# Optimization experiments

Measured on AMD Instinct MI355X. Metric: run time of the kernel, lower is better.

Reference implementation:

```python
import jax, jax.numpy as jnp
import numpy as np

BN_EPS = 1e-5
N_NODES = 100000
N_EDGES = 1600000
IN_DIM = 128
HID = 256   # 2 * out_dim
OUT_DIM = 128


def setup_inputs() -> dict:
    key = jax.random.key(0)
    ks = jax.random.split(key, 8)
    x = jax.random.normal(ks[0], (N_NODES, IN_DIM), dtype=jnp.float32)
    edge_index = jax.random.randint(ks[1], (2, N_EDGES), 0, N_NODES, dtype=jnp.int32)
    # GINConv learned eps (train_eps=True), init 0
    eps = jnp.zeros((), dtype=jnp.float32)
    # MLP: Linear(in, 2*out) -> BN -> ReLU -> Linear(2*out, out)
    s1 = 1.0 / np.sqrt(IN_DIM)
    s2 = 1.0 / np.sqrt(HID)
    W1 = jax.random.uniform(ks[2], (IN_DIM, HID), jnp.float32, -s1, s1)
    b1 = jax.random.uniform(ks[3], (HID,), jnp.float32, -s1, s1)
    g1 = jnp.ones((HID,), jnp.float32)
    beta1 = jnp.zeros((HID,), jnp.float32)
    W2 = jax.random.uniform(ks[4], (HID, OUT_DIM), jnp.float32, -s2, s2)
    b2 = jax.random.uniform(ks[5], (OUT_DIM,), jnp.float32, -s2, s2)
    # outer BatchNorm
    g2 = jnp.ones((OUT_DIM,), jnp.float32)
    beta2 = jnp.zeros((OUT_DIM,), jnp.float32)
    return {"x": x, "edge_index": edge_index, "eps": eps,
            "W1": W1, "b1": b1, "g1": g1, "beta1": beta1,
            "W2": W2, "b2": b2, "g2": g2, "beta2": beta2}


def _batchnorm(h, gamma, beta):
    # training-mode BatchNorm1d: batch mean, biased variance
    mu = jnp.mean(h, axis=0)
    var = jnp.mean(jnp.square(h - mu), axis=0)
    return (h - mu) * jax.lax.rsqrt(var + BN_EPS) * gamma + beta


def reference(x, edge_index, eps, W1, b1, g1, beta1, W2, b2, g2, beta2):
    src, dst = edge_index[0], edge_index[1]
    # sum-aggregation of neighbor features: scatter-add x[src] onto dst
    aggr = jax.ops.segment_sum(x[src], dst, num_segments=x.shape[0])  # [N, in_dim]
    h = (1.0 + eps) * x + aggr
    # MLP: Linear -> BN -> ReLU -> Linear
    h = h @ W1 + b1
    h = jax.nn.relu(_batchnorm(h, g1, beta1))
    h = h @ W2 + b2
    # outer BN + ReLU
    return jax.nn.relu(_batchnorm(h, g2, beta2))
```

## Files before the change

### kernel.cpp

```cpp
#include <hip/hip_runtime.h>
#include <hip/hip_bf16.h>

#define N_NODES 100000
#define N_EDGES 1600000
#define IN_DIM  128
#define HID     256
#define OUT_DIM 128
#define BN_EPS  1e-5f

typedef unsigned int u32;
typedef unsigned short u16;
typedef __attribute__((ext_vector_type(8))) short short8v;
typedef __attribute__((ext_vector_type(4))) float f32x4;

__device__ __forceinline__ float bf2f(u16 h) {
    return __uint_as_float(((u32)h) << 16);
}
__device__ __forceinline__ u16 f2bf(float f) {
    u32 u = __float_as_uint(f);
    u32 r = (u + 0x7fffu + ((u >> 16) & 1u)) >> 16;
    return (u16)r;
}
__device__ __forceinline__ u32 pack2(float a, float b) {
    return (u32)f2bf(a) | ((u32)f2bf(b) << 16);
}
__device__ __forceinline__ void gload16(const void* g, void* l) {
    __builtin_amdgcn_global_load_lds((const __attribute__((address_space(1))) u32*)g,
                                     (__attribute__((address_space(3))) u32*)l, 16, 0, 0);
}
#define MFMA(a,b,c) __builtin_amdgcn_mfma_f32_16x16x32_bf16(a, b, c, 0, 0, 0)

__global__ __launch_bounds__(256) void k_prep(const float* __restrict__ x,
                                              const int* __restrict__ ei,
                                              const float* __restrict__ W1,
                                              const float* __restrict__ W2,
                                              uint2* __restrict__ xb,
                                              int* __restrict__ head2,
                                              int2* __restrict__ nxt,
                                              char* __restrict__ w1t,
                                              char* __restrict__ w2t) {
    int t = blockIdx.x * 256 + threadIdx.x;
    {
        float4 v = ((const float4*)x)[t];
        uint2 p;
        p.x = pack2(v.x, v.y);
        p.y = pack2(v.z, v.w);
        xb[t] = p;
    }
    if (t < N_EDGES) {
        int dst = ei[N_EDGES + t];
        int src = ei[t];
        int old = atomicExch(&head2[dst * 2 + (t & 1)], t);
        nxt[t] = make_int2(old, src);
    }
    if (t < 8192) {
        u16 tmp[8];
        if (t < 4096) {
            int j = t >> 4, kc = t & 15;
            #pragma unroll
            for (int i = 0; i < 8; ++i) tmp[i] = f2bf(W1[(kc * 8 + i) * HID + j]);
            u32 off = ((u32)(j * 256 + kc * 16)) ^ (((u32)(j & 7)) << 4);
            uint4 q;
            q.x = (u32)tmp[0] | ((u32)tmp[1] << 16);
            q.y = (u32)tmp[2] | ((u32)tmp[3] << 16);
            q.z = (u32)tmp[4] | ((u32)tmp[5] << 16);
            q.w = (u32)tmp[6] | ((u32)tmp[7] << 16);
            *(uint4*)(w1t + off) = q;
        } else {
            int t2 = t - 4096;
            int j = t2 >> 5, kc = t2 & 31;
            #pragma unroll
            for (int i = 0; i < 8; ++i) tmp[i] = f2bf(W2[(kc * 8 + i) * OUT_DIM + j]);
            u32 off = ((u32)(j * 512 + kc * 16)) ^ (((u32)(j & 7)) << 4);
            uint4 q;
            q.x = (u32)tmp[0] | ((u32)tmp[1] << 16);
            q.y = (u32)tmp[2] | ((u32)tmp[3] << 16);
            q.z = (u32)tmp[4] | ((u32)tmp[5] << 16);
            q.w = (u32)tmp[6] | ((u32)tmp[7] << 16);
            *(uint4*)(w2t + off) = q;
        }
    }
}

__global__ __launch_bounds__(256) void k_aggregate(const uint4* __restrict__ xb4,
                                                   const int2* __restrict__ nxt,
                                                   const int* __restrict__ head2,
                                                   const float* __restrict__ epsp,
                                                   char* __restrict__ aggrb) {
    const int lane = threadIdx.x & 63;
    const int w = threadIdx.x >> 6;
    const int q = lane >> 4, l = lane & 15;
    const int nq = q >> 1, p = q & 1;
    const int node = blockIdx.x * 8 + w * 2 + nq;

    float a[8];
    #pragma unroll
    for (int i = 0; i < 8; ++i) a[i] = 0.f;

    if (p == 0) {
        float sc = 1.0f + epsp[0];
        uint4 v = xb4[node * 16 + l];
        a[0] = bf2f((u16)v.x) * sc;  a[1] = bf2f((u16)(v.x >> 16)) * sc;
        a[2] = bf2f((u16)v.y) * sc;  a[3] = bf2f((u16)(v.y >> 16)) * sc;
        a[4] = bf2f((u16)v.z) * sc;  a[5] = bf2f((u16)(v.z >> 16)) * sc;
        a[6] = bf2f((u16)v.w) * sc;  a[7] = bf2f((u16)(v.w >> 16)) * sc;
    }
    int e = head2[node * 2 + p];
    while (e >= 0) {
        int2 nv = nxt[e];
        e = nv.x;
        uint4 v = xb4[nv.y * 16 + l];
        a[0] += bf2f((u16)v.x);  a[1] += bf2f((u16)(v.x >> 16));
        a[2] += bf2f((u16)v.y);  a[3] += bf2f((u16)(v.y >> 16));
        a[4] += bf2f((u16)v.z);  a[5] += bf2f((u16)(v.z >> 16));
        a[6] += bf2f((u16)v.w);  a[7] += bf2f((u16)(v.w >> 16));
    }
    #pragma unroll
    for (int i = 0; i < 8; ++i) a[i] += __shfl_xor(a[i], 16);
    if (p == 0) {
        uint4 o;
        o.x = pack2(a[0], a[1]);
        o.y = pack2(a[2], a[3]);
        o.z = pack2(a[4], a[5]);
        o.w = pack2(a[6], a[7]);
        u32 b = ((u32)node * 256 + (u32)l * 16) ^ (((u32)(node & 7)) << 4);
        *(uint4*)(aggrb + b) = o;
    }
}

__global__ __launch_bounds__(512) void k_gemm1(const char* __restrict__ aggrb,
                                               const char* __restrict__ w1t,
                                               const float* __restrict__ b1,
                                               u16* __restrict__ h1t,
                                               float* __restrict__ gstats) {
    __shared__ u16 Als[160 * 128];
    __shared__ u16 Bls[256 * 128];
    __shared__ float slds[512];

    const int tid = threadIdx.x, lane = tid & 63, w = tid >> 6;
    const int wr = w >> 2, wc = w & 3;
    const int base = blockIdx.x * 160;

    slds[tid] = 0.f;

    char* lA = (char*)Als;
    char* lB = (char*)Bls;
    const char* ga = aggrb + (size_t)base * 256;
    #pragma unroll
    for (int i = 0; i < 5; ++i)
        gload16(ga + i * 8192 + w * 1024 + (lane << 4), lA + i * 8192 + w * 1024);
    #pragma unroll
    for (int i = 0; i < 8; ++i)
        gload16(w1t + i * 8192 + w * 1024 + (lane << 4), lB + i * 8192 + w * 1024);

    const int rA = lane & 15;
    const int q = lane >> 4;
    const int kb = q << 3;
    const u32 xsw = ((u32)(rA & 7)) << 4;
    int colv[4]; float bcol[4];
    #pragma unroll
    for (int n = 0; n < 4; ++n) { colv[n] = wc * 64 + n * 16 + rA; bcol[n] = b1[colv[n]]; }

    asm volatile("s_waitcnt vmcnt(0)" ::: "memory");
    __syncthreads();

    f32x4 acc[5][4];
    #pragma unroll
    for (int m = 0; m < 5; ++m)
        #pragma unroll
        for (int n = 0; n < 4; ++n) acc[m][n] = (f32x4){0.f, 0.f, 0.f, 0.f};

    #pragma unroll
    for (int ks = 0; ks < 4; ++ks) {
        const int kk2 = (ks * 32 + kb) * 2;
        short8v a[5], b[4];
        #pragma unroll
        for (int m = 0; m < 5; ++m) {
            u32 off = ((u32)((wr * 80 + m * 16 + rA) * 256 + kk2)) ^ xsw;
            a[m] = *(const short8v*)(lA + off);
        }
        #pragma unroll
        for (int n = 0; n < 4; ++n) {
            u32 off = ((u32)(colv[n] * 256 + kk2)) ^ xsw;
            b[n] = *(const short8v*)(lB + off);
        }
        #pragma unroll
        for (int m = 0; m < 5; ++m)
            #pragma unroll
            for (int n = 0; n < 4; ++n)
                acc[m][n] = MFMA(a[m], b[n], acc[m][n]);
    }

    const int Tb = blockIdx.x * 10 + wr * 5;
    float csum[4] = {0.f,0.f,0.f,0.f}, csq[4] = {0.f,0.f,0.f,0.f};
    #pragma unroll
    for (int m = 0; m < 5; ++m) {
        int T = Tb + m;
        #pragma unroll
        for (int n = 0; n < 4; ++n) {
            f32x4 d = acc[m][n];
            float v0 = d[0] + bcol[n], v1 = d[1] + bcol[n];
            float v2 = d[2] + bcol[n], v3 = d[3] + bcol[n];
            csum[n] += v0 + v1 + v2 + v3;
            csq[n]  += v0*v0 + v1*v1 + v2*v2 + v3*v3;
            uint2 p; p.x = pack2(v0, v1); p.y = pack2(v2, v3);
            *(uint2*)(h1t + (size_t)T * 4096 + colv[n] * 16 + q * 4) = p;
        }
    }
    #pragma unroll
    for (int n = 0; n < 4; ++n) {
        csum[n] += __shfl_xor(csum[n], 16); csum[n] += __shfl_xor(csum[n], 32);
        csq[n]  += __shfl_xor(csq[n], 16);  csq[n]  += __shfl_xor(csq[n], 32);
    }
    if (lane < 16) {
        #pragma unroll
        for (int n = 0; n < 4; ++n) {
            atomicAdd(&slds[colv[n]], csum[n]);
            atomicAdd(&slds[256 + colv[n]], csq[n]);
        }
    }
    __syncthreads();
    atomicAdd(&gstats[tid], slds[tid]);
}

__global__ __launch_bounds__(512) void k_gemm2(const uint4* __restrict__ h1t4,
                                               const char* __restrict__ w2t,
                                               const float* __restrict__ b2,
                                               const float* __restrict__ g1,
                                               const float* __restrict__ beta1,
                                               const float* __restrict__ gstats,
                                               u16* __restrict__ h2t,
                                               float* __restrict__ gstats2) {
    __shared__ u16 Als[160 * 128];
    __shared__ u16 Bls[128 * 256];
    __shared__ float a1s[256], b1s[256];
    __shared__ float slds[256];

    const int tid = threadIdx.x, lane = tid & 63, w = tid >> 6;
    const int wr = w >> 2, wc = w & 3;
    const int Tbase = blockIdx.x * 10;

    if (tid < 256) {
        float s = gstats[tid], sq = gstats[256 + tid];
        float mu = s * (1.0f / N_NODES);
        float var = sq * (1.0f / N_NODES) - mu * mu;
        float inv = rsqrtf(var + BN_EPS);
        float a = g1[tid] * inv;
        a1s[tid] = a;
        b1s[tid] = beta1[tid] - mu * a;
        slds[tid] = 0.f;
    }

    char* lA = (char*)Als;
    char* lB = (char*)Bls;
    #pragma unroll
    for (int i = 0; i < 8; ++i)
        gload16(w2t + i * 8192 + w * 1024 + (lane << 4), lB + i * 8192 + w * 1024);

    const int rA = lane & 15;
    const int q = lane >> 4;
    const int kb = q << 3;
    const u32 xsw = ((u32)(rA & 7)) << 4;
    int colv[2]; float bcol[2];
    #pragma unroll
    for (int n = 0; n < 2; ++n) { colv[n] = wc * 32 + n * 16 + rA; bcol[n] = b2[colv[n]]; }

    __syncthreads();

    f32x4 acc[5][2];
    #pragma unroll
    for (int m = 0; m < 5; ++m)
        #pragma unroll
        for (int n = 0; n < 2; ++n) acc[m][n] = (f32x4){0.f, 0.f, 0.f, 0.f};

    for (int kh = 0; kh < 2; ++kh) {
        #pragma unroll
        for (int i = 0; i < 5; ++i) {
            int id = i * 512 + tid;
            int kl = id & 127;
            int h16 = (id >> 7) & 1;
            int Tl = id >> 8;
            int kg = kh * 128 + kl;
            uint4 v = h1t4[(size_t)(Tbase + Tl) * 512 + kg * 2 + h16];
            float a = a1s[kg], b = b1s[kg];
            int r0 = Tl * 16 + h16 * 8;
            u16 hv[8] = {(u16)v.x, (u16)(v.x >> 16), (u16)v.y, (u16)(v.y >> 16),
                         (u16)v.z, (u16)(v.z >> 16), (u16)v.w, (u16)(v.w >> 16)};
            #pragma unroll
            for (int rr = 0; rr < 8; ++rr) {
                float f = fmaxf(bf2f(hv[rr]) * a + b, 0.f);
                int r = r0 + rr;
                u32 off = ((u32)(r * 256 + kl * 2)) ^ (((u32)(r & 7)) << 4);
                *(u16*)(lA + off) = f2bf(f);
            }
        }
        if (kh == 0) asm volatile("s_waitcnt vmcnt(0)" ::: "memory");
        __syncthreads();

        #pragma unroll
        for (int ks = 0; ks < 4; ++ks) {
            const int kk2 = (ks * 32 + kb) * 2;
            short8v a[5], b[2];
            #pragma unroll
            for (int n = 0; n < 2; ++n) {
                u32 off = ((u32)(colv[n] * 512 + kh * 256 + kk2)) ^ xsw;
                b[n] = *(const short8v*)(lB + off);
            }
            #pragma unroll
            for (int m = 0; m < 5; ++m) {
                u32 off = ((u32)((wr * 80 + m * 16 + rA) * 256 + kk2)) ^ xsw;
                a[m] = *(const short8v*)(lA + off);
            }
            #pragma unroll
            for (int m = 0; m < 5; ++m)
                #pragma unroll
                for (int n = 0; n < 2; ++n)
                    acc[m][n] = MFMA(a[m], b[n], acc[m][n]);
        }
        __syncthreads();
    }

    const int Tb = Tbase + wr * 5;
    float csum[2] = {0.f,0.f}, csq[2] = {0.f,0.f};
    #pragma unroll
    for (int m = 0; m < 5; ++m) {
        int T = Tb + m;
        #pragma unroll
        for (int n = 0; n < 2; ++n) {
            f32x4 d = acc[m][n];
            float v0 = d[0] + bcol[n], v1 = d[1] + bcol[n];
            float v2 = d[2] + bcol[n], v3 = d[3] + bcol[n];
            csum[n] += v0 + v1 + v2 + v3;
            csq[n]  += v0*v0 + v1*v1 + v2*v2 + v3*v3;
            uint2 p; p.x = pack2(v0, v1); p.y = pack2(v2, v3);
            *(uint2*)(h2t + (size_t)T * 2048 + colv[n] * 16 + q * 4) = p;
        }
    }
    #pragma unroll
    for (int n = 0; n < 2; ++n) {
        csum[n] += __shfl_xor(csum[n], 16); csum[n] += __shfl_xor(csum[n], 32);
        csq[n]  += __shfl_xor(csq[n], 16);  csq[n]  += __shfl_xor(csq[n], 32);
    }
    if (lane < 16) {
        #pragma unroll
        for (int n = 0; n < 2; ++n) {
            atomicAdd(&slds[colv[n]], csum[n]);
            atomicAdd(&slds[128 + colv[n]], csq[n]);
        }
    }
    __syncthreads();
    if (tid < 256) atomicAdd(&gstats2[tid], slds[tid]);
}

__global__ __launch_bounds__(256) void k_bn2(const uint4* __restrict__ h2t4,
                                             float* __restrict__ out,
                                             const float* __restrict__ gstats2,
                                             const float* __restrict__ g2,
                                             const float* __restrict__ beta2) {
    __shared__ float fl[32 * 128];
    __shared__ float a2s[128], b2s[128];
    const int tid = threadIdx.x;
    if (tid < 128) {
        float s = gstats2[tid], sq = gstats2[128 + tid];
        float mu = s * (1.0f / N_NODES);
        float var = sq * (1.0f / N_NODES) - mu * mu;
        float inv = rsqrtf(var + BN_EPS);
        float a = g2[tid] * inv;
        a2s[tid] = a;
        b2s[tid] = beta2[tid] - mu * a;
    }
    __syncthreads();
    const int Tbase = blockIdx.x * 2;
    #pragma unroll
    for (int i = 0; i < 2; ++i) {
        int id = i * 256 + tid;
        int kl = id & 127;
        int h16 = (id >> 7) & 1;
        int Tl = id >> 8;
        uint4 v = h2t4[(size_t)(Tbase + Tl) * 256 + kl * 2 + h16];
        float a = a2s[kl], b = b2s[kl];
        int r0 = Tl * 16 + h16 * 8;
        u16 hv[8] = {(u16)v.x, (u16)(v.x >> 16), (u16)v.y, (u16)(v.y >> 16),
                     (u16)v.z, (u16)(v.z >> 16), (u16)v.w, (u16)(v.w >> 16)};
        #pragma unroll
        for (int rr = 0; rr < 8; ++rr)
            fl[(r0 + rr) * 128 + kl] = fmaxf(bf2f(hv[rr]) * a + b, 0.f);
    }
    __syncthreads();
    #pragma unroll
    for (int i = 0; i < 4; ++i) {
        int id = i * 256 + tid;
        int row = id >> 5;
        int ch = id & 31;
        float4 vv = *(const float4*)&fl[row * 128 + ch * 4];
        ((float4*)out)[(size_t)(blockIdx.x * 32 + row) * 32 + ch] = vv;
    }
}

extern "C" void kernel_launch(void* const* d_in, const int* in_sizes, int n_in,
                              void* d_out, int out_size, void* d_ws, size_t ws_size,
                              hipStream_t stream) {
    const float* x     = (const float*)d_in[0];
    const int*   ei    = (const int*)d_in[1];
    const float* epsp  = (const float*)d_in[2];
    const float* W1    = (const float*)d_in[3];
    const float* b1    = (const float*)d_in[4];
    const float* g1    = (const float*)d_in[5];
    const float* beta1 = (const float*)d_in[6];
    const float* W2    = (const float*)d_in[7];
    const float* b2    = (const float*)d_in[8];
    const float* g2    = (const float*)d_in[9];
    const float* beta2 = (const float*)d_in[10];

    char* ws = (char*)d_ws;
    char*  aggrb   = ws;
    u16*   h2t     = (u16*)ws;
    u16*   h1t     = (u16*)(ws + 25600000);
    int2*  nxt     = (int2*)(ws + 25600000);
    int*   head2   = (int*)(ws + 38400000);
    uint2* xb      = (uint2*)(ws + 39200000);
    float* gstats  = (float*)(ws + 76800000);
    float* gstats2 = gstats + 512;
    char*  w1t     = ws + 76804096;
    char*  w2t     = ws + 76869632;
    float* out = (float*)d_out;

    hipMemsetAsync(head2, 0xFF, 800000, stream);
    hipMemsetAsync(gstats, 0, 768 * sizeof(float), stream);

    k_prep<<<12500, 256, 0, stream>>>(x, ei, W1, W2, xb, head2, nxt, w1t, w2t);
    k_aggregate<<<N_NODES / 8, 256, 0, stream>>>((const uint4*)xb, nxt, head2, epsp, aggrb);
    k_gemm1<<<625, 512, 0, stream>>>(aggrb, w1t, b1, h1t, gstats);
    k_gemm2<<<625, 512, 0, stream>>>((const uint4*)h1t, w2t, b2, g1, beta1, gstats, h2t, gstats2);
    k_bn2<<<3125, 256, 0, stream>>>((const uint4*)h2t, out, gstats2, g2, beta2);
}
```

Before: 257.0 us.

## Halve GEMM weight LDS via K-split loads, restructure aggregation, fold stats memset

Weight tiles in both GEMM kernels are now staged into LDS in two K-halves instead of all at once. This halves the B buffer, so more blocks can be resident per CU, at the cost of an extra barrier and a serialized weight load per half. The aggregation kernel now assigns one 16-lane group per node, which walks both edge lists with two interleaved chains, removing the cross-group shuffle and halving thread count. Zeroing of the BN stats buffer moves into the prep kernel, removing one memset launch.

```diff
diff --git a/kernel.cpp b/kernel.cpp
--- a/kernel.cpp
+++ b/kernel.cpp
@@ -38,7 +38,8 @@
                                               int* __restrict__ head2,
                                               int2* __restrict__ nxt,
                                               char* __restrict__ w1t,
-                                              char* __restrict__ w2t) {
+                                              char* __restrict__ w2t,
+                                              float* __restrict__ gstats) {
     int t = blockIdx.x * 256 + threadIdx.x;
     {
         float4 v = ((const float4*)x)[t];
@@ -53,6 +54,7 @@
         int old = atomicExch(&head2[dst * 2 + (t & 1)], t);
         nxt[t] = make_int2(old, src);
     }
+    if (t < 768) gstats[t] = 0.f;
     if (t < 8192) {
         u16 tmp[8];
         if (t < 4096) {
@@ -87,45 +89,60 @@
                                                    const int* __restrict__ head2,
                                                    const float* __restrict__ epsp,
                                                    char* __restrict__ aggrb) {
-    const int lane = threadIdx.x & 63;
-    const int w = threadIdx.x >> 6;
-    const int q = lane >> 4, l = lane & 15;
-    const int nq = q >> 1, p = q & 1;
-    const int node = blockIdx.x * 8 + w * 2 + nq;
-
+    const int tid = threadIdx.x;
+    const int l = tid & 15;
+    const int node = blockIdx.x * 16 + (tid >> 4);
+
+    const float sc = 1.0f + epsp[0];
+    uint4 v = xb4[node * 16 + l];
     float a[8];
-    #pragma unroll
-    for (int i = 0; i < 8; ++i) a[i] = 0.f;
-
-    if (p == 0) {
-        float sc = 1.0f + epsp[0];
-        uint4 v = xb4[node * 16 + l];
-        a[0] = bf2f((u16)v.x) * sc;  a[1] = bf2f((u16)(v.x >> 16)) * sc;
-        a[2] = bf2f((u16)v.y) * sc;  a[3] = bf2f((u16)(v.y >> 16)) * sc;
-        a[4] = bf2f((u16)v.z) * sc;  a[5] = bf2f((u16)(v.z >> 16)) * sc;
-        a[6] = bf2f((u16)v.w) * sc;  a[7] = bf2f((u16)(v.w >> 16)) * sc;
-    }
-    int e = head2[node * 2 + p];
-    while (e >= 0) {
-        int2 nv = nxt[e];
-        e = nv.x;
-        uint4 v = xb4[nv.y * 16 + l];
-        a[0] += bf2f((u16)v.x);  a[1] += bf2f((u16)(v.x >> 16));
-        a[2] += bf2f((u16)v.y);  a[3] += bf2f((u16)(v.y >> 16));
-        a[4] += bf2f((u16)v.z);  a[5] += bf2f((u16)(v.z >> 16));
-        a[6] += bf2f((u16)v.w);  a[7] += bf2f((u16)(v.w >> 16));
-    }
-    #pragma unroll
-    for (int i = 0; i < 8; ++i) a[i] += __shfl_xor(a[i], 16);
-    if (p == 0) {
-        uint4 o;
-        o.x = pack2(a[0], a[1]);
-        o.y = pack2(a[2], a[3]);
-        o.z = pack2(a[4], a[5]);
-        o.w = pack2(a[6], a[7]);
-        u32 b = ((u32)node * 256 + (u32)l * 16) ^ (((u32)(node & 7)) << 4);
-        *(uint4*)(aggrb + b) = o;
-    }
+    a[0] = bf2f((u16)v.x) * sc;  a[1] = bf2f((u16)(v.x >> 16)) * sc;
+    a[2] = bf2f((u16)v.y) * sc;  a[3] = bf2f((u16)(v.y >> 16)) * sc;
+    a[4] = bf2f((u16)v.z) * sc;  a[5] = bf2f((u16)(v.z >> 16)) * sc;
+    a[6] = bf2f((u16)v.w) * sc;  a[7] = bf2f((u16)(v.w >> 16)) * sc;
+
+    int e0 = head2[node * 2];
+    int e1 = head2[node * 2 + 1];
+    while (e0 >= 0 && e1 >= 0) {
+        int2 n0 = nxt[e0];
+        int2 n1 = nxt[e1];
+        uint4 v0 = xb4[n0.y * 16 + l];
+        uint4 v1 = xb4[n1.y * 16 + l];
+        e0 = n0.x; e1 = n1.x;
+        a[0] += bf2f((u16)v0.x);  a[1] += bf2f((u16)(v0.x >> 16));
+        a[2] += bf2f((u16)v0.y);  a[3] += bf2f((u16)(v0.y >> 16));
+        a[4] += bf2f((u16)v0.z);  a[5] += bf2f((u16)(v0.z >> 16));
+        a[6] += bf2f((u16)v0.w);  a[7] += bf2f((u16)(v0.w >> 16));
+        a[0] += bf2f((u16)v1.x);  a[1] += bf2f((u16)(v1.x >> 16));
+        a[2] += bf2f((u16)v1.y);  a[3] += bf2f((u16)(v1.y >> 16));
+        a[4] += bf2f((u16)v1.z);  a[5] += bf2f((u16)(v1.z >> 16));
+        a[6] += bf2f((u16)v1.w);  a[7] += bf2f((u16)(v1.w >> 16));
+    }
+    while (e0 >= 0) {
+        int2 n0 = nxt[e0];
+        uint4 v0 = xb4[n0.y * 16 + l];
+        e0 = n0.x;
+        a[0] += bf2f((u16)v0.x);  a[1] += bf2f((u16)(v0.x >> 16));
+        a[2] += bf2f((u16)v0.y);  a[3] += bf2f((u16)(v0.y >> 16));
+        a[4] += bf2f((u16)v0.z);  a[5] += bf2f((u16)(v0.z >> 16));
+        a[6] += bf2f((u16)v0.w);  a[7] += bf2f((u16)(v0.w >> 16));
+    }
+    while (e1 >= 0) {
+        int2 n1 = nxt[e1];
+        uint4 v1 = xb4[n1.y * 16 + l];
+        e1 = n1.x;
+        a[0] += bf2f((u16)v1.x);  a[1] += bf2f((u16)(v1.x >> 16));
+        a[2] += bf2f((u16)v1.y);  a[3] += bf2f((u16)(v1.y >> 16));
+        a[4] += bf2f((u16)v1.z);  a[5] += bf2f((u16)(v1.z >> 16));
+        a[6] += bf2f((u16)v1.w);  a[7] += bf2f((u16)(v1.w >> 16));
+    }
+    uint4 o;
+    o.x = pack2(a[0], a[1]);
+    o.y = pack2(a[2], a[3]);
+    o.z = pack2(a[4], a[5]);
+    o.w = pack2(a[6], a[7]);
+    u32 b = ((u32)node * 256 + (u32)l * 16) ^ (((u32)(node & 7)) << 4);
+    *(uint4*)(aggrb + b) = o;
 }
 
 __global__ __launch_bounds__(512) void k_gemm1(const char* __restrict__ aggrb,
@@ -134,7 +151,7 @@
                                                u16* __restrict__ h1t,
                                                float* __restrict__ gstats) {
     __shared__ u16 Als[160 * 128];
-    __shared__ u16 Bls[256 * 128];
+    __shared__ u16 Bls[256 * 64];
     __shared__ float slds[512];
 
     const int tid = threadIdx.x, lane = tid & 63, w = tid >> 6;
@@ -149,9 +166,6 @@
     #pragma unroll
     for (int i = 0; i < 5; ++i)
         gload16(ga + i * 8192 + w * 1024 + (lane << 4), lA + i * 8192 + w * 1024);
-    #pragma unroll
-    for (int i = 0; i < 8; ++i)
-        gload16(w1t + i * 8192 + w * 1024 + (lane << 4), lB + i * 8192 + w * 1024);
 
     const int rA = lane & 15;
     const int q = lane >> 4;
@@ -161,34 +175,45 @@
     #pragma unroll
     for (int n = 0; n < 4; ++n) { colv[n] = wc * 64 + n * 16 + rA; bcol[n] = b1[colv[n]]; }
 
-    asm volatile("s_waitcnt vmcnt(0)" ::: "memory");
-    __syncthreads();
-
     f32x4 acc[5][4];
     #pragma unroll
     for (int m = 0; m < 5; ++m)
         #pragma unroll
         for (int n = 0; n < 4; ++n) acc[m][n] = (f32x4){0.f, 0.f, 0.f, 0.f};
 
-    #pragma unroll
-    for (int ks = 0; ks < 4; ++ks) {
-        const int kk2 = (ks * 32 + kb) * 2;
-        short8v a[5], b[4];
-        #pragma unroll
-        for (int m = 0; m < 5; ++m) {
-            u32 off = ((u32)((wr * 80 + m * 16 + rA) * 256 + kk2)) ^ xsw;
-            a[m] = *(const short8v*)(lA + off);
-        }
-        #pragma unroll
-        for (int n = 0; n < 4; ++n) {
-            u32 off = ((u32)(colv[n] * 256 + kk2)) ^ xsw;
-            b[n] = *(const short8v*)(lB + off);
-        }
-        #pragma unroll
-        for (int m = 0; m < 5; ++m)
-            #pragma unroll
-            for (int n = 0; n < 4; ++n)
-                acc[m][n] = MFMA(a[m], b[n], acc[m][n]);
+    for (int kh = 0; kh < 2; ++kh) {
+        if (kh) __syncthreads();
+        #pragma unroll
+        for (int i = 0; i < 4; ++i) {
+            int idx = i * 512 + tid;
+            int j = idx >> 3, kc8 = idx & 7;
+            u32 src = (u32)j * 256 + (u32)kh * 128 + (u32)kc8 * 16;
+            gload16(w1t + src, lB + idx * 16);
+        }
+        asm volatile("s_waitcnt vmcnt(0)" ::: "memory");
+        __syncthreads();
+
+        #pragma unroll
+        for (int ksl = 0; ksl < 2; ++ksl) {
+            const int kk2A = (kh * 64 + ksl * 32 + kb) * 2;
+            const int kk2B = (ksl * 32 + kb) * 2;
+            short8v a[5], b[4];
+            #pragma unroll
+            for (int m = 0; m < 5; ++m) {
+                u32 off = ((u32)((wr * 80 + m * 16 + rA) * 256 + kk2A)) ^ xsw;
+                a[m] = *(const short8v*)(lA + off);
+            }
+            #pragma unroll
+            for (int n = 0; n < 4; ++n) {
+                u32 off = ((u32)(colv[n] * 128 + kk2B)) ^ xsw;
+                b[n] = *(const short8v*)(lB + off);
+            }
+            #pragma unroll
+            for (int m = 0; m < 5; ++m)
+                #pragma unroll
+                for (int n = 0; n < 4; ++n)
+                    acc[m][n] = MFMA(a[m], b[n], acc[m][n]);
+        }
     }
 
     const int Tb = blockIdx.x * 10 + wr * 5;
@@ -232,7 +257,7 @@
                                                u16* __restrict__ h2t,
                                                float* __restrict__ gstats2) {
     __shared__ u16 Als[160 * 128];
-    __shared__ u16 Bls[128 * 256];
+    __shared__ u16 Bls[128 * 128];
     __shared__ float a1s[256], b1s[256];
     __shared__ float slds[256];
 
@@ -253,9 +278,6 @@
 
     char* lA = (char*)Als;
     char* lB = (char*)Bls;
-    #pragma unroll
-    for (int i = 0; i < 8; ++i)
-        gload16(w2t + i * 8192 + w * 1024 + (lane << 4), lB + i * 8192 + w * 1024);
 
     const int rA = lane & 15;
     const int q = lane >> 4;
@@ -294,7 +316,14 @@
                 *(u16*)(lA + off) = f2bf(f);
             }
         }
-        if (kh == 0) asm volatile("s_waitcnt vmcnt(0)" ::: "memory");
+        #pragma unroll
+        for (int i = 0; i < 4; ++i) {
+            int idx = i * 512 + tid;
+            int j = idx >> 4, kc16 = idx & 15;
+            u32 src = (u32)j * 512 + (u32)kh * 256 + (u32)kc16 * 16;
+            gload16(w2t + src, lB + idx * 16);
+        }
+        asm volatile("s_waitcnt vmcnt(0)" ::: "memory");
         __syncthreads();
 
         #pragma unroll
@@ -303,7 +332,7 @@
             short8v a[5], b[2];
             #pragma unroll
             for (int n = 0; n < 2; ++n) {
-                u32 off = ((u32)(colv[n] * 512 + kh * 256 + kk2)) ^ xsw;
+                u32 off = ((u32)(colv[n] * 256 + kk2)) ^ xsw;
                 b[n] = *(const short8v*)(lB + off);
             }
             #pragma unroll
@@ -426,10 +455,9 @@
     float* out = (float*)d_out;
 
     hipMemsetAsync(head2, 0xFF, 800000, stream);
-    hipMemsetAsync(gstats, 0, 768 * sizeof(float), stream);
-
-    k_prep<<<12500, 256, 0, stream>>>(x, ei, W1, W2, xb, head2, nxt, w1t, w2t);
-    k_aggregate<<<N_NODES / 8, 256, 0, stream>>>((const uint4*)xb, nxt, head2, epsp, aggrb);
+
+    k_prep<<<12500, 256, 0, stream>>>(x, ei, W1, W2, xb, head2, nxt, w1t, w2t, gstats);
+    k_aggregate<<<N_NODES / 16, 256, 0, stream>>>((const uint4*)xb, nxt, head2, epsp, aggrb);
     k_gemm1<<<625, 512, 0, stream>>>(aggrb, w1t, b1, h1t, gstats);
     k_gemm2<<<625, 512, 0, stream>>>((const uint4*)h1t, w2t, b2, g1, beta1, gstats, h2t, gstats2);
     k_bn2<<<3125, 256, 0, stream>>>((const uint4*)h2t, out, gstats2, g2, beta2);
```

Measured after the change: 253.3 us. Within noise of the previous version (-1.4%).

## Halve GEMM tiles and stage weights in K-chunks for higher occupancy

Applied to the files above, without the earlier changes.

Both GEMM kernels drop from 160-row tiles with 512 threads to 80-row tiles with 256 threads and twice as many blocks. The weight matrix is now staged through LDS in K-chunks, which shrinks shared memory so more blocks fit per CU, with launch_bounds occupancy hints added. Block-level LDS stat reduction is replaced by direct global atomics, and the gstats memset moves into k_prep. In exchange there are more barriers, repeated weight loads per block, and more global atomic traffic.

```diff
diff --git a/kernel.cpp b/kernel.cpp
--- a/kernel.cpp
+++ b/kernel.cpp
@@ -38,7 +38,8 @@
                                               int* __restrict__ head2,
                                               int2* __restrict__ nxt,
                                               char* __restrict__ w1t,
-                                              char* __restrict__ w2t) {
+                                              char* __restrict__ w2t,
+                                              float* __restrict__ gstats) {
     int t = blockIdx.x * 256 + threadIdx.x;
     {
         float4 v = ((const float4*)x)[t];
@@ -53,6 +54,7 @@
         int old = atomicExch(&head2[dst * 2 + (t & 1)], t);
         nxt[t] = make_int2(old, src);
     }
+    if (t < 768) gstats[t] = 0.f;
     if (t < 8192) {
         u16 tmp[8];
         if (t < 4096) {
@@ -128,70 +130,72 @@
     }
 }
 
-__global__ __launch_bounds__(512) void k_gemm1(const char* __restrict__ aggrb,
-                                               const char* __restrict__ w1t,
-                                               const float* __restrict__ b1,
-                                               u16* __restrict__ h1t,
-                                               float* __restrict__ gstats) {
-    __shared__ u16 Als[160 * 128];
-    __shared__ u16 Bls[256 * 128];
-    __shared__ float slds[512];
-
-    const int tid = threadIdx.x, lane = tid & 63, w = tid >> 6;
-    const int wr = w >> 2, wc = w & 3;
-    const int base = blockIdx.x * 160;
-
-    slds[tid] = 0.f;
-
-    char* lA = (char*)Als;
-    char* lB = (char*)Bls;
-    const char* ga = aggrb + (size_t)base * 256;
-    #pragma unroll
-    for (int i = 0; i < 5; ++i)
-        gload16(ga + i * 8192 + w * 1024 + (lane << 4), lA + i * 8192 + w * 1024);
-    #pragma unroll
-    for (int i = 0; i < 8; ++i)
-        gload16(w1t + i * 8192 + w * 1024 + (lane << 4), lB + i * 8192 + w * 1024);
-
+__global__ __launch_bounds__(256, 3) void k_gemm1(const char* __restrict__ aggrb,
+                                                  const char* __restrict__ w1t,
+                                                  const float* __restrict__ b1,
+                                                  u16* __restrict__ h1t,
+                                                  float* __restrict__ gstats) {
+    __shared__ u16 Als[80 * 128];
+    __shared__ u16 Bls[256 * 64];
+
+    const int tid = threadIdx.x, lane = tid & 63, wc = tid >> 6;
     const int rA = lane & 15;
     const int q = lane >> 4;
     const int kb = q << 3;
     const u32 xsw = ((u32)(rA & 7)) << 4;
+
+    char* lA = (char*)Als;
+    char* lB = (char*)Bls;
+    const char* ga = aggrb + (size_t)blockIdx.x * 20480;
+    #pragma unroll
+    for (int i = 0; i < 5; ++i)
+        gload16(ga + (i * 256 + tid) * 16, lA + (i * 256 + tid) * 16);
+
     int colv[4]; float bcol[4];
     #pragma unroll
     for (int n = 0; n < 4; ++n) { colv[n] = wc * 64 + n * 16 + rA; bcol[n] = b1[colv[n]]; }
 
-    asm volatile("s_waitcnt vmcnt(0)" ::: "memory");
-    __syncthreads();
-
     f32x4 acc[5][4];
     #pragma unroll
     for (int m = 0; m < 5; ++m)
         #pragma unroll
         for (int n = 0; n < 4; ++n) acc[m][n] = (f32x4){0.f, 0.f, 0.f, 0.f};
 
-    #pragma unroll
-    for (int ks = 0; ks < 4; ++ks) {
-        const int kk2 = (ks * 32 + kb) * 2;
-        short8v a[5], b[4];
-        #pragma unroll
-        for (int m = 0; m < 5; ++m) {
-            u32 off = ((u32)((wr * 80 + m * 16 + rA) * 256 + kk2)) ^ xsw;
-            a[m] = *(const short8v*)(lA + off);
-        }
-        #pragma unroll
-        for (int n = 0; n < 4; ++n) {
-            u32 off = ((u32)(colv[n] * 256 + kk2)) ^ xsw;
-            b[n] = *(const short8v*)(lB + off);
-        }
-        #pragma unroll
-        for (int m = 0; m < 5; ++m)
-            #pragma unroll
-            for (int n = 0; n < 4; ++n)
-                acc[m][n] = MFMA(a[m], b[n], acc[m][n]);
-    }
-
-    const int Tb = blockIdx.x * 10 + wr * 5;
+    for (int kh = 0; kh < 2; ++kh) {
+        if (kh) __syncthreads();
+        #pragma unroll
+        for (int i = 0; i < 8; ++i) {
+            int idx = i * 256 + tid;
+            int j = idx >> 3, kc8 = idx & 7;
+            gload16(w1t + (u32)j * 256 + (u32)kh * 128 + (u32)kc8 * 16, lB + idx * 16);
+        }
+        asm volatile("s_waitcnt vmcnt(0)" ::: "memory");
+        __syncthreads();
+
+        #pragma unroll
+        for (int ksl = 0; ksl < 2; ++ksl) {
+            const int kk2A = (kh * 64 + ksl * 32 + kb) * 2;
+            const int kk2B = (ksl * 32 + kb) * 2;
+            short8v a[5], b[4];
+            #pragma unroll
+            for (int m = 0; m < 5; ++m) {
+                u32 off = ((u32)((m * 16 + rA) * 256 + kk2A)) ^ xsw;
+                a[m] = *(const short8v*)(lA + off);
+            }
+            #pragma unroll
+            for (int n = 0; n < 4; ++n) {
+                u32 off = ((u32)(colv[n] * 128 + kk2B)) ^ xsw;
+                b[n] = *(const short8v*)(lB + off);
+            }
+            #pragma unroll
+            for (int m = 0; m < 5; ++m)
+                #pragma unroll
+                for (int n = 0; n < 4; ++n)
+                    acc[m][n] = MFMA(a[m], b[n], acc[m][n]);
+        }
+    }
+
+    const int Tb = blockIdx.x * 5;
     float csum[4] = {0.f,0.f,0.f,0.f}, csq[4] = {0.f,0.f,0.f,0.f};
     #pragma unroll
     for (int m = 0; m < 5; ++m) {
@@ -215,32 +219,32 @@
     if (lane < 16) {
         #pragma unroll
         for (int n = 0; n < 4; ++n) {
-            atomicAdd(&slds[colv[n]], csum[n]);
-            atomicAdd(&slds[256 + colv[n]], csq[n]);
-        }
-    }
-    __syncthreads();
-    atomicAdd(&gstats[tid], slds[tid]);
-}
-
-__global__ __launch_bounds__(512) void k_gemm2(const uint4* __restrict__ h1t4,
-                                               const char* __restrict__ w2t,
-                                               const float* __restrict__ b2,
-                                               const float* __restrict__ g1,
-                                               const float* __restrict__ beta1,
-                                               const float* __restrict__ gstats,
-                                               u16* __restrict__ h2t,
-                                               float* __restrict__ gstats2) {
-    __shared__ u16 Als[160 * 128];
-    __shared__ u16 Bls[128 * 256];
+            atomicAdd(&gstats[colv[n]], csum[n]);
+            atomicAdd(&gstats[256 + colv[n]], csq[n]);
+        }
+    }
+}
+
+__global__ __launch_bounds__(256, 4) void k_gemm2(const uint4* __restrict__ h1t4,
+                                                  const char* __restrict__ w2t,
+                                                  const float* __restrict__ b2,
+                                                  const float* __restrict__ g1,
+                                                  const float* __restrict__ beta1,
+                                                  const float* __restrict__ gstats,
+                                                  u16* __restrict__ h2t,
+                                                  float* __restrict__ gstats2) {
+    __shared__ u16 Als[80 * 128];
+    __shared__ u16 Bls[128 * 64];
     __shared__ float a1s[256], b1s[256];
-    __shared__ float slds[256];
-
-    const int tid = threadIdx.x, lane = tid & 63, w = tid >> 6;
-    const int wr = w >> 2, wc = w & 3;
-    const int Tbase = blockIdx.x * 10;
-
-    if (tid < 256) {
+
+    const int tid = threadIdx.x, lane = tid & 63, wc = tid >> 6;
+    const int rA = lane & 15;
+    const int q = lane >> 4;
+    const int kb = q << 3;
+    const u32 xsw = ((u32)(rA & 7)) << 4;
+    const int Tbase = blockIdx.x * 5;
+
+    {
         float s = gstats[tid], sq = gstats[256 + tid];
         float mu = s * (1.0f / N_NODES);
         float var = sq * (1.0f / N_NODES) - mu * mu;
@@ -248,19 +252,10 @@
         float a = g1[tid] * inv;
         a1s[tid] = a;
         b1s[tid] = beta1[tid] - mu * a;
-        slds[tid] = 0.f;
     }
 
     char* lA = (char*)Als;
     char* lB = (char*)Bls;
-    #pragma unroll
-    for (int i = 0; i < 8; ++i)
-        gload16(w2t + i * 8192 + w * 1024 + (lane << 4), lB + i * 8192 + w * 1024);
-
-    const int rA = lane & 15;
-    const int q = lane >> 4;
-    const int kb = q << 3;
-    const u32 xsw = ((u32)(rA & 7)) << 4;
     int colv[2]; float bcol[2];
     #pragma unroll
     for (int n = 0; n < 2; ++n) { colv[n] = wc * 32 + n * 16 + rA; bcol[n] = b2[colv[n]]; }
@@ -276,7 +271,7 @@
     for (int kh = 0; kh < 2; ++kh) {
         #pragma unroll
         for (int i = 0; i < 5; ++i) {
-            int id = i * 512 + tid;
+            int id = i * 256 + tid;
             int kl = id & 127;
             int h16 = (id >> 7) & 1;
             int Tl = id >> 8;
@@ -294,37 +289,46 @@
                 *(u16*)(lA + off) = f2bf(f);
             }
         }
-        if (kh == 0) asm volatile("s_waitcnt vmcnt(0)" ::: "memory");
-        __syncthreads();
-
-        #pragma unroll
-        for (int ks = 0; ks < 4; ++ks) {
-            const int kk2 = (ks * 32 + kb) * 2;
-            short8v a[5], b[2];
-            #pragma unroll
-            for (int n = 0; n < 2; ++n) {
-                u32 off = ((u32)(colv[n] * 512 + kh * 256 + kk2)) ^ xsw;
-                b[n] = *(const short8v*)(lB + off);
+        for (int kq = 0; kq < 2; ++kq) {
+            #pragma unroll
+            for (int i = 0; i < 4; ++i) {
+                int idx = i * 256 + tid;
+                int j = idx >> 3, kc8 = idx & 7;
+                gload16(w2t + (u32)j * 512 + (u32)(kh * 2 + kq) * 128 + (u32)kc8 * 16,
+                        lB + idx * 16);
             }
-            #pragma unroll
-            for (int m = 0; m < 5; ++m) {
-                u32 off = ((u32)((wr * 80 + m * 16 + rA) * 256 + kk2)) ^ xsw;
-                a[m] = *(const short8v*)(lA + off);
+            asm volatile("s_waitcnt vmcnt(0)" ::: "memory");
+            __syncthreads();
+
+            #pragma unroll
+            for (int ks = 0; ks < 2; ++ks) {
+                const int kk2A = (kq * 64 + ks * 32 + kb) * 2;
+                const int kk2B = (ks * 32 + kb) * 2;
+                short8v a[5], b[2];
+                #pragma unroll
+                for (int n = 0; n < 2; ++n) {
+                    u32 off = ((u32)(colv[n] * 128 + kk2B)) ^ xsw;
+                    b[n] = *(const short8v*)(lB + off);
+                }
+                #pragma unroll
+                for (int m = 0; m < 5; ++m) {
+                    u32 off = ((u32)((m * 16 + rA) * 256 + kk2A)) ^ xsw;
+                    a[m] = *(const short8v*)(lA + off);
+                }
+                #pragma unroll
+                for (int m = 0; m < 5; ++m)
+                    #pragma unroll
+                    for (int n = 0; n < 2; ++n)
+                        acc[m][n] = MFMA(a[m], b[n], acc[m][n]);
             }
-            #pragma unroll
-            for (int m = 0; m < 5; ++m)
-                #pragma unroll
-                for (int n = 0; n < 2; ++n)
-                    acc[m][n] = MFMA(a[m], b[n], acc[m][n]);
-        }
-        __syncthreads();
-    }
-
-    const int Tb = Tbase + wr * 5;
+            __syncthreads();
+        }
+    }
+
     float csum[2] = {0.f,0.f}, csq[2] = {0.f,0.f};
     #pragma unroll
     for (int m = 0; m < 5; ++m) {
-        int T = Tb + m;
+        int T = Tbase + m;
         #pragma unroll
         for (int n = 0; n < 2; ++n) {
             f32x4 d = acc[m][n];
@@ -344,12 +348,10 @@
     if (lane < 16) {
         #pragma unroll
         for (int n = 0; n < 2; ++n) {
-            atomicAdd(&slds[colv[n]], csum[n]);
-            atomicAdd(&slds[128 + colv[n]], csq[n]);
-        }
-    }
-    __syncthreads();
-    if (tid < 256) atomicAdd(&gstats2[tid], slds[tid]);
+            atomicAdd(&gstats2[colv[n]], csum[n]);
+            atomicAdd(&gstats2[128 + colv[n]], csq[n]);
+        }
+    }
 }
 
 __global__ __launch_bounds__(256) void k_bn2(const uint4* __restrict__ h2t4,
@@ -426,11 +428,10 @@
     float* out = (float*)d_out;
 
     hipMemsetAsync(head2, 0xFF, 800000, stream);
-    hipMemsetAsync(gstats, 0, 768 * sizeof(float), stream);
-
-    k_prep<<<12500, 256, 0, stream>>>(x, ei, W1, W2, xb, head2, nxt, w1t, w2t);
+
+    k_prep<<<12500, 256, 0, stream>>>(x, ei, W1, W2, xb, head2, nxt, w1t, w2t, gstats);
     k_aggregate<<<N_NODES / 8, 256, 0, stream>>>((const uint4*)xb, nxt, head2, epsp, aggrb);
-    k_gemm1<<<625, 512, 0, stream>>>(aggrb, w1t, b1, h1t, gstats);
-    k_gemm2<<<625, 512, 0, stream>>>((const uint4*)h1t, w2t, b2, g1, beta1, gstats, h2t, gstats2);
+    k_gemm1<<<1250, 256, 0, stream>>>(aggrb, w1t, b1, h1t, gstats);
+    k_gemm2<<<1250, 256, 0, stream>>>((const uint4*)h1t, w2t, b2, g1, beta1, gstats, h2t, gstats2);
     k_bn2<<<3125, 256, 0, stream>>>((const uint4*)h2t, out, gstats2, g2, beta2);
 }
```

New measurement: 298.2 us. 1.16x slower.

## Read GEMM weight tiles directly from global memory and fold stats zeroing into prep

Applied to the files above, without the earlier changes.

Both GEMM kernels stop staging the bf16 weight matrices in LDS and read B fragments straight from global memory (L2/L1-cached), so the weight layout drops its XOR swizzle. This cuts LDS use per block (64KB less), which may allow more resident blocks, and removes the bulk weight copy at the start of each block. In exchange, every MFMA step issues global loads with higher latency. The zeroing of the BN statistics buffer moves from a separate memset into the prep kernel, removing one launch.

```diff
diff --git a/kernel.cpp b/kernel.cpp
--- a/kernel.cpp
+++ b/kernel.cpp
@@ -38,7 +38,8 @@
                                               int* __restrict__ head2,
                                               int2* __restrict__ nxt,
                                               char* __restrict__ w1t,
-                                              char* __restrict__ w2t) {
+                                              char* __restrict__ w2t,
+                                              float* __restrict__ gstats) {
     int t = blockIdx.x * 256 + threadIdx.x;
     {
         float4 v = ((const float4*)x)[t];
@@ -53,13 +54,14 @@
         int old = atomicExch(&head2[dst * 2 + (t & 1)], t);
         nxt[t] = make_int2(old, src);
     }
+    if (t < 768) gstats[t] = 0.f;
     if (t < 8192) {
         u16 tmp[8];
         if (t < 4096) {
             int j = t >> 4, kc = t & 15;
             #pragma unroll
             for (int i = 0; i < 8; ++i) tmp[i] = f2bf(W1[(kc * 8 + i) * HID + j]);
-            u32 off = ((u32)(j * 256 + kc * 16)) ^ (((u32)(j & 7)) << 4);
+            u32 off = (u32)(j * 256 + kc * 16);
             uint4 q;
             q.x = (u32)tmp[0] | ((u32)tmp[1] << 16);
             q.y = (u32)tmp[2] | ((u32)tmp[3] << 16);
@@ -71,7 +73,7 @@
             int j = t2 >> 5, kc = t2 & 31;
             #pragma unroll
             for (int i = 0; i < 8; ++i) tmp[i] = f2bf(W2[(kc * 8 + i) * OUT_DIM + j]);
-            u32 off = ((u32)(j * 512 + kc * 16)) ^ (((u32)(j & 7)) << 4);
+            u32 off = (u32)(j * 512 + kc * 16);
             uint4 q;
             q.x = (u32)tmp[0] | ((u32)tmp[1] << 16);
             q.y = (u32)tmp[2] | ((u32)tmp[3] << 16);
@@ -134,7 +136,6 @@
                                                u16* __restrict__ h1t,
                                                float* __restrict__ gstats) {
     __shared__ u16 Als[160 * 128];
-    __shared__ u16 Bls[256 * 128];
     __shared__ float slds[512];
 
     const int tid = threadIdx.x, lane = tid & 63, w = tid >> 6;
@@ -144,14 +145,10 @@
     slds[tid] = 0.f;
 
     char* lA = (char*)Als;
-    char* lB = (char*)Bls;
     const char* ga = aggrb + (size_t)base * 256;
     #pragma unroll
     for (int i = 0; i < 5; ++i)
         gload16(ga + i * 8192 + w * 1024 + (lane << 4), lA + i * 8192 + w * 1024);
-    #pragma unroll
-    for (int i = 0; i < 8; ++i)
-        gload16(w1t + i * 8192 + w * 1024 + (lane << 4), lB + i * 8192 + w * 1024);
 
     const int rA = lane & 15;
     const int q = lane >> 4;
@@ -175,14 +172,12 @@
         const int kk2 = (ks * 32 + kb) * 2;
         short8v a[5], b[4];
         #pragma unroll
+        for (int n = 0; n < 4; ++n)
+            b[n] = *(const short8v*)(w1t + colv[n] * 256 + kk2);
+        #pragma unroll
         for (int m = 0; m < 5; ++m) {
             u32 off = ((u32)((wr * 80 + m * 16 + rA) * 256 + kk2)) ^ xsw;
             a[m] = *(const short8v*)(lA + off);
-        }
-        #pragma unroll
-        for (int n = 0; n < 4; ++n) {
-            u32 off = ((u32)(colv[n] * 256 + kk2)) ^ xsw;
-            b[n] = *(const short8v*)(lB + off);
         }
         #pragma unroll
         for (int m = 0; m < 5; ++m)
@@ -232,7 +227,6 @@
                                                u16* __restrict__ h2t,
                                                float* __restrict__ gstats2) {
     __shared__ u16 Als[160 * 128];
-    __shared__ u16 Bls[128 * 256];
     __shared__ float a1s[256], b1s[256];
     __shared__ float slds[256];
 
@@ -252,10 +246,6 @@
     }
 
     char* lA = (char*)Als;
-    char* lB = (char*)Bls;
-    #pragma unroll
-    for (int i = 0; i < 8; ++i)
-        gload16(w2t + i * 8192 + w * 1024 + (lane << 4), lB + i * 8192 + w * 1024);
 
     const int rA = lane & 15;
     const int q = lane >> 4;
@@ -274,6 +264,7 @@
         for (int n = 0; n < 2; ++n) acc[m][n] = (f32x4){0.f, 0.f, 0.f, 0.f};
 
     for (int kh = 0; kh < 2; ++kh) {
+        if (kh) __syncthreads();
         #pragma unroll
         for (int i = 0; i < 5; ++i) {
             int id = i * 512 + tid;
@@ -294,7 +285,6 @@
                 *(u16*)(lA + off) = f2bf(f);
             }
         }
-        if (kh == 0) asm volatile("s_waitcnt vmcnt(0)" ::: "memory");
         __syncthreads();
 
         #pragma unroll
@@ -302,10 +292,8 @@
             const int kk2 = (ks * 32 + kb) * 2;
             short8v a[5], b[2];
             #pragma unroll
-            for (int n = 0; n < 2; ++n) {
-                u32 off = ((u32)(colv[n] * 512 + kh * 256 + kk2)) ^ xsw;
-                b[n] = *(const short8v*)(lB + off);
-            }
+            for (int n = 0; n < 2; ++n)
+                b[n] = *(const short8v*)(w2t + colv[n] * 512 + kh * 256 + kk2);
             #pragma unroll
             for (int m = 0; m < 5; ++m) {
                 u32 off = ((u32)((wr * 80 + m * 16 + rA) * 256 + kk2)) ^ xsw;
@@ -317,7 +305,6 @@
                 for (int n = 0; n < 2; ++n)
                     acc[m][n] = MFMA(a[m], b[n], acc[m][n]);
         }
-        __syncthreads();
     }
 
     const int Tb = Tbase + wr * 5;
@@ -426,9 +413,8 @@
     float* out = (float*)d_out;
 
     hipMemsetAsync(head2, 0xFF, 800000, stream);
-    hipMemsetAsync(gstats, 0, 768 * sizeof(float), stream);
-
-    k_prep<<<12500, 256, 0, stream>>>(x, ei, W1, W2, xb, head2, nxt, w1t, w2t);
+
+    k_prep<<<12500, 256, 0, stream>>>(x, ei, W1, W2, xb, head2, nxt, w1t, w2t, gstats);
     k_aggregate<<<N_NODES / 8, 256, 0, stream>>>((const uint4*)xb, nxt, head2, epsp, aggrb);
     k_gemm1<<<625, 512, 0, stream>>>(aggrb, w1t, b1, h1t, gstats);
     k_gemm2<<<625, 512, 0, stream>>>((const uint4*)h1t, w2t, b2, g1, beta1, gstats, h2t, gstats2);
```

After: 261.6 us. Within noise of the previous version (+1.8%).
